# Performance work log

Hardware: AMD Instinct MI355X
Metric: run time of the kernel (lower is better)

## Reference

```python
import jax, jax.numpy as jnp
import numpy as np
import math

S, B, D = 2048, 8, 256
HEADS = 8
DPROJ = 128
DFF = 1024
DH = DPROJ // HEADS  # 16


def _layernorm(x, g, b, eps=1e-5):
    mu = jnp.mean(x, axis=-1, keepdims=True)
    var = jnp.mean((x - mu) ** 2, axis=-1, keepdims=True)
    return (x - mu) * jax.lax.rsqrt(var + eps) * g + b


def setup_inputs() -> dict:
    key = jax.random.key(0)
    ks = jax.random.split(key, 16)
    s = 0.02
    return {
        "src": jax.random.normal(ks[0], (S, B, D), dtype=jnp.float32),
        "Wq": jax.random.normal(ks[1], (D, DPROJ), dtype=jnp.float32) * s,
        "bq": jnp.zeros((DPROJ,), dtype=jnp.float32),
        "Wk": jax.random.normal(ks[2], (D, DPROJ), dtype=jnp.float32) * s,
        "bk": jnp.zeros((DPROJ,), dtype=jnp.float32),
        "Wv": jax.random.normal(ks[3], (D, DPROJ), dtype=jnp.float32) * s,
        "bv": jnp.zeros((DPROJ,), dtype=jnp.float32),
        "Wo": jax.random.normal(ks[4], (DPROJ, D), dtype=jnp.float32) * s,
        "ln1_g": jnp.ones((D,), dtype=jnp.float32),
        "ln1_b": jnp.zeros((D,), dtype=jnp.float32),
        "W1": jax.random.normal(ks[5], (D, DFF), dtype=jnp.float32) * s,
        "b1": jnp.zeros((DFF,), dtype=jnp.float32),
        "W2": jax.random.normal(ks[6], (DFF, D), dtype=jnp.float32) * s,
        "b2": jnp.zeros((D,), dtype=jnp.float32),
        "ln2_g": jnp.ones((D,), dtype=jnp.float32),
        "ln2_b": jnp.zeros((D,), dtype=jnp.float32),
    }


def reference(src, Wq, bq, Wk, bk, Wv, bv, Wo, ln1_g, ln1_b, W1, b1, W2, b2, ln2_g, ln2_b):
    # src: (S, B, D)
    q = src @ Wq + bq  # (S, B, DPROJ)
    k = src @ Wk + bk
    v = src @ Wv + bv

    # _reshape_to_batches: (S, B, h*dh) -> (S, B*h, dh), then sdpa moves batch first
    def split_heads(x):
        return jnp.transpose(x.reshape(S, B * HEADS, DH), (1, 0, 2))  # (B*h, S, dh)

    qh, kh, vh = split_heads(q), split_heads(k), split_heads(v)
    scores = jnp.einsum('bid,bjd->bij', qh, kh) / math.sqrt(DH)  # (B*h, S, S)
    attn = jax.nn.softmax(scores, axis=-1)
    ctx = jnp.einsum('bij,bjd->bid', attn, vh)  # (B*h, S, dh)

    # _reshape_from_batches: (B*h, S, dh) -> (S, B, DPROJ)
    ctx = jnp.transpose(ctx, (1, 0, 2)).reshape(S, B, DPROJ)
    y = ctx @ Wo  # (S, B, D), no bias

    x = _layernorm(src + y, ln1_g, ln1_b)
    ffn = jax.nn.relu(x @ W1 + b1) @ W2 + b2
    return _layernorm(x + ffn, ln2_g, ln2_b)
```

## Files before the change

kernel.cpp:

```cpp
#include <hip/hip_runtime.h>
#include <math.h>

#define SLEN 2048
#define BATCH 8
#define DMODEL 256
#define HEADS 8
#define DPROJ 128
#define DFF 1024
#define DH 16
#define MROWS (SLEN*BATCH)

typedef unsigned short u16;
typedef unsigned int u32;
typedef __attribute__((ext_vector_type(8))) short short8;
typedef __attribute__((ext_vector_type(4))) float f32x4;
typedef __attribute__((ext_vector_type(4))) unsigned short u16x4;

__device__ __forceinline__ u16 f2bf(float x) {
    union { float f; u32 u; } v; v.f = x;
    u32 r = v.u + 0x7FFFu + ((v.u >> 16) & 1u);
    return (u16)(r >> 16);
}
__device__ __forceinline__ float bf2f(u16 h) {
    union { u32 u; float f; } v; v.u = ((u32)h) << 16;
    return v.f;
}
__device__ __forceinline__ float fexp2(float x) { return __builtin_amdgcn_exp2f(x); }
__device__ __forceinline__ u32 pack_bf(float lo, float hi) {
    union { float f; u32 u; } a, b; a.f = lo; b.f = hi;
    return __builtin_amdgcn_perm(b.u, a.u, 0x07060302u);
}
__device__ __forceinline__ void gld16(const u16* g, u16* l) {
    __builtin_amdgcn_global_load_lds(
        (const __attribute__((address_space(1))) void*)g,
        (__attribute__((address_space(3))) void*)l, 16, 0, 0);
}

__global__ void prep_kernel(const float* __restrict__ src, u16* __restrict__ srcb,
                            const float* __restrict__ Wq, const float* __restrict__ Wk,
                            const float* __restrict__ Wv, const float* __restrict__ Wo,
                            const float* __restrict__ W1, const float* __restrict__ W2,
                            u16* __restrict__ WqT, u16* __restrict__ WkT,
                            u16* __restrict__ WvT, u16* __restrict__ WoT,
                            u16* __restrict__ W1T, u16* __restrict__ W2T) {
    if (blockIdx.x < 4096) {
        int idx = (blockIdx.x * 256 + threadIdx.x) * 4;
        float4 v = *(const float4*)(src + idx);
        u16x4 o;
        o.x = f2bf(v.x); o.y = f2bf(v.y); o.z = f2bf(v.z); o.w = f2bf(v.w);
        *(u16x4*)(srcb + idx) = o;
        return;
    }
    int i = (blockIdx.x - 4096) * 256 + threadIdx.x;
    if (i < 32768) {
        int n = i >> 8, k = i & 255;
        WqT[i] = f2bf(Wq[k * 128 + n]);
    } else if (i < 65536) {
        int j = i - 32768; int n = j >> 8, k = j & 255;
        WkT[j] = f2bf(Wk[k * 128 + n]);
    } else if (i < 98304) {
        int j = i - 65536; int n = j >> 8, k = j & 255;
        WvT[j] = f2bf(Wv[k * 128 + n]);
    } else if (i < 131072) {
        int j = i - 98304; int n = j >> 7, k = j & 127;
        WoT[j] = f2bf(Wo[k * 256 + n]);
    } else if (i < 393216) {
        int j = i - 131072; int n = j >> 8, k = j & 255;
        W1T[j] = f2bf(W1[k * 1024 + n]);
    } else if (i < 655360) {
        int j = i - 393216; int n = j >> 10, k = j & 1023;
        W2T[j] = f2bf(W2[k * 256 + n]);
    }
}

template<int BN, bool RELU, bool HAS_BIAS, bool OUT_BF16>
__global__ void mfma_gemm(const u16* __restrict__ A, const u16* __restrict__ BT,
                          const float* __restrict__ bias, void* __restrict__ Cout,
                          int M, int N, int K) {
    constexpr int NJ = BN / 32;
    __shared__ __align__(16) u16 As[128 * 32];
    __shared__ __align__(16) u16 Bs[BN * 32];
    const int tid = threadIdx.x;
    const int row0 = blockIdx.x * 128;
    const int col0 = blockIdx.y * BN;
    const int w = tid >> 6, l = tid & 63;
    const int wr = (w & 1) * 64, wc = (w >> 1) * (BN / 2);
    const int lcol = l & 15, lrow = (l >> 4) * 4, g = l >> 4;
    const int sl = l >> 2;
    const int swc = ((l & 3) ^ (sl & 3)) * 8;
    const int fsw = (g ^ (lcol & 3)) * 8;

    const u16* Ag0 = A + (size_t)(row0 + 16 * w + sl) * K + swc;
    const u16* Ag1 = Ag0 + (size_t)64 * K;
    const u16* Bg0 = BT + (size_t)(col0 + 16 * w + sl) * K + swc;
    const u16* Bg1 = Bg0 + (size_t)64 * K;
    u16* lA0 = As + (16 * w) * 32;
    u16* lA1 = As + (16 * w + 64) * 32;
    u16* lB0 = Bs + (16 * w) * 32;
    u16* lB1 = Bs + (16 * w + 64) * 32;

    f32x4 acc[4][NJ] = {};
    for (int k0 = 0; k0 < K; k0 += 32) {
        gld16(Ag0 + k0, lA0);
        gld16(Ag1 + k0, lA1);
        gld16(Bg0 + k0, lB0);
        if (BN == 128) gld16(Bg1 + k0, lB1);
        __syncthreads();
        short8 af[4], bf[NJ];
        #pragma unroll
        for (int i = 0; i < 4; ++i)
            af[i] = *(const short8*)(As + (wr + i * 16 + lcol) * 32 + fsw);
        #pragma unroll
        for (int j = 0; j < NJ; ++j)
            bf[j] = *(const short8*)(Bs + (wc + j * 16 + lcol) * 32 + fsw);
        #pragma unroll
        for (int i = 0; i < 4; ++i)
            #pragma unroll
            for (int j = 0; j < NJ; ++j)
                acc[i][j] = __builtin_amdgcn_mfma_f32_16x16x32_bf16(
                    af[i], bf[j], acc[i][j], 0, 0, 0);
        __syncthreads();
    }
    float bv[NJ];
    #pragma unroll
    for (int j = 0; j < NJ; ++j)
        bv[j] = HAS_BIAS ? bias[col0 + wc + j * 16 + lcol] : 0.f;
    #pragma unroll
    for (int i = 0; i < 4; ++i) {
        #pragma unroll
        for (int r = 0; r < 4; ++r) {
            size_t grow = row0 + wr + i * 16 + lrow + r;
            #pragma unroll
            for (int j = 0; j < NJ; ++j) {
                int gcol = col0 + wc + j * 16 + lcol;
                float c = acc[i][j][r] + bv[j];
                if (RELU) c = fmaxf(c, 0.f);
                if (OUT_BF16) ((u16*)Cout)[grow * N + gcol] = f2bf(c);
                else          ((float*)Cout)[grow * N + gcol] = c;
            }
        }
    }
}

__global__ void qkv_mfma(const u16* __restrict__ A,
                         const u16* __restrict__ WqT, const u16* __restrict__ WkT,
                         const u16* __restrict__ WvT,
                         const float* __restrict__ bq, const float* __restrict__ bk,
                         const float* __restrict__ bv,
                         u16* __restrict__ qhp, u16* __restrict__ khp,
                         u16* __restrict__ vhb) {
    const int which = blockIdx.z;
    const u16* BT   = which == 0 ? WqT : (which == 1 ? WkT : WvT);
    const float* bs = which == 0 ? bq : (which == 1 ? bk : bv);
    const float scale = which == 0 ? 0.25f * 1.44269504f : 1.0f;
    __shared__ __align__(16) u16 As[128 * 32];
    __shared__ __align__(16) u16 Bs[128 * 32];
    const int tid = threadIdx.x;
    const int row0 = blockIdx.x * 128;
    const int w = tid >> 6, l = tid & 63;
    const int wr = (w & 1) * 64, wc = (w >> 1) * 64;
    const int lcol = l & 15, lrow = (l >> 4) * 4, g = l >> 4;
    const int sl = l >> 2;
    const int swc = ((l & 3) ^ (sl & 3)) * 8;
    const int fsw = (g ^ (lcol & 3)) * 8;

    const u16* Ag0 = A + (size_t)(row0 + 16 * w + sl) * DMODEL + swc;
    const u16* Ag1 = Ag0 + (size_t)64 * DMODEL;
    const u16* Bg0 = BT + (size_t)(16 * w + sl) * DMODEL + swc;
    const u16* Bg1 = Bg0 + (size_t)64 * DMODEL;
    u16* lA0 = As + (16 * w) * 32;
    u16* lA1 = As + (16 * w + 64) * 32;
    u16* lB0 = Bs + (16 * w) * 32;
    u16* lB1 = Bs + (16 * w + 64) * 32;

    f32x4 acc[4][4] = {};
    for (int k0 = 0; k0 < DMODEL; k0 += 32) {
        gld16(Ag0 + k0, lA0);
        gld16(Ag1 + k0, lA1);
        gld16(Bg0 + k0, lB0);
        gld16(Bg1 + k0, lB1);
        __syncthreads();
        short8 af[4], bf[4];
        #pragma unroll
        for (int i = 0; i < 4; ++i)
            af[i] = *(const short8*)(As + (wr + i * 16 + lcol) * 32 + fsw);
        #pragma unroll
        for (int j = 0; j < 4; ++j)
            bf[j] = *(const short8*)(Bs + (wc + j * 16 + lcol) * 32 + fsw);
        #pragma unroll
        for (int i = 0; i < 4; ++i)
            #pragma unroll
            for (int j = 0; j < 4; ++j)
                acc[i][j] = __builtin_amdgcn_mfma_f32_16x16x32_bf16(
                    af[i], bf[j], acc[i][j], 0, 0, 0);
        __syncthreads();
    }
    #pragma unroll
    for (int i = 0; i < 4; ++i) {
        #pragma unroll
        for (int r = 0; r < 4; ++r) {
            int grow = row0 + wr + i * 16 + lrow + r;
            int b = grow & 7, s = grow >> 3;
            #pragma unroll
            for (int j = 0; j < 4; ++j) {
                int gcol = wc + j * 16 + lcol;
                int h = gcol >> 4, d = gcol & 15;
                float c = acc[i][j][r] + bs[gcol];
                if (which == 2) {
                    vhb[((size_t)(b * 8 + h) * SLEN + s) * 16 + d] = f2bf(c);
                } else {
                    u16* base = (which == 0 ? qhp : khp)
                              + ((size_t)(b * 8 + h) * SLEN + s) * 32;
                    base[d] = f2bf(c * scale);
                    base[d + 16] = 0;
                }
            }
        }
    }
}

__global__ void transpose_v(const u16* __restrict__ vhb, u16* __restrict__ vT) {
    __shared__ u16 T[128 * 24];
    const int bh = blockIdx.y;
    const int c0 = blockIdx.x * 128;
    const int t = threadIdx.x;
    {
        int key = t >> 1, half = t & 1;
        *(uint4*)(T + key * 24 + half * 8) =
            *(const uint4*)(vhb + ((size_t)bh * SLEN + c0 + key) * 16 + half * 8);
    }
    __syncthreads();
    int d = t >> 4, k8 = (t & 15) * 8;
    u16x4 o0, o1;
    o0.x = T[(k8 + 0) * 24 + d]; o0.y = T[(k8 + 1) * 24 + d];
    o0.z = T[(k8 + 2) * 24 + d]; o0.w = T[(k8 + 3) * 24 + d];
    o1.x = T[(k8 + 4) * 24 + d]; o1.y = T[(k8 + 5) * 24 + d];
    o1.z = T[(k8 + 6) * 24 + d]; o1.w = T[(k8 + 7) * 24 + d];
    u16* dst = vT + ((size_t)bh * 16 + d) * SLEN + c0 + k8;
    *(u16x4*)dst = o0;
    *(u16x4*)(dst + 4) = o1;
}

__global__ __launch_bounds__(256, 4)
void attn_mfma(const u16* __restrict__ qg, const u16* __restrict__ kg,
               const u16* __restrict__ vT, u16* __restrict__ ctx) {
    __shared__ __align__(16) u16 Ps[2 * 4 * 32 * 76];
    const int bh = blockIdx.y;
    const int q0 = blockIdx.x * 128;
    const int tid = threadIdx.x;
    const int w = tid >> 6, l = tid & 63;
    const int qc = l & 15, g = l >> 4;
    u16* Pw0 = Ps + w * 2432;
    u16* Pw1 = Ps + 9728 + w * 2432;

    short8 qf[2];
    {
        const u16* qbase = qg + ((size_t)bh * SLEN + q0 + w * 32) * 32;
        qf[0] = *(const short8*)(qbase + qc * 32 + 8 * g);
        qf[1] = *(const short8*)(qbase + (16 + qc) * 32 + 8 * g);
    }
    const u16* kbase = kg + (size_t)bh * SLEN * 32;
    const u16* vbase = vT + ((size_t)bh * 16 + qc) * SLEN;

    f32x4 o_[2] = {};
    f32x4 ls[2] = {};
    const short one_bf = (short)0x3F80;
    short8 onesB = {one_bf, one_bf, one_bf, one_bf, one_bf, one_bf, one_bf, one_bf};

    #pragma unroll 2
    for (int kt = 0; kt < 32; ++kt) {
        const int k0 = kt * 64;
        u16* Pw = (kt & 1) ? Pw1 : Pw0;
        short8 kf[4], vf[2];
        #pragma unroll
        for (int kj = 0; kj < 4; ++kj)
            kf[kj] = *(const short8*)(kbase + (size_t)(k0 + kj * 16 + qc) * 32 + 8 * g);
        #pragma unroll
        for (int ks = 0; ks < 2; ++ks)
            vf[ks] = *(const short8*)(vbase + k0 + ks * 32 + 8 * g);

        f32x4 s_[4][2];
        #pragma unroll
        for (int kj = 0; kj < 4; ++kj)
            #pragma unroll
            for (int mi = 0; mi < 2; ++mi) {
                f32x4 z = {0.f, 0.f, 0.f, 0.f};
                s_[kj][mi] = __builtin_amdgcn_mfma_f32_16x16x32_bf16(
                    kf[kj], qf[mi], z, 0, 0, 0);
            }
        #pragma unroll
        for (int mi = 0; mi < 2; ++mi)
            #pragma unroll
            for (int kj = 0; kj < 4; ++kj) {
                f32x4 sv = s_[kj][mi];
                uint2 dd;
                dd.x = pack_bf(fexp2(sv[0]), fexp2(sv[1]));
                dd.y = pack_bf(fexp2(sv[2]), fexp2(sv[3]));
                *(uint2*)(Pw + (mi * 16 + qc) * 76 + kj * 16 + 4 * g) = dd;
            }
        #pragma unroll
        for (int ks = 0; ks < 2; ++ks) {
            #pragma unroll
            for (int mi = 0; mi < 2; ++mi) {
                const u16* rp = Pw + (mi * 16 + qc) * 76 + ks * 32 + 8 * g;
                union { uint2 q[2]; short8 v; } ap;
                ap.q[0] = *(const uint2*)rp;
                ap.q[1] = *(const uint2*)(rp + 4);
                o_[mi] = __builtin_amdgcn_mfma_f32_16x16x32_bf16(ap.v, vf[ks], o_[mi], 0, 0, 0);
                ls[mi] = __builtin_amdgcn_mfma_f32_16x16x32_bf16(ap.v, onesB, ls[mi], 0, 0, 0);
            }
        }
    }
    const int b = bh >> 3, h = bh & 7;
    #pragma unroll
    for (int mi = 0; mi < 2; ++mi)
        #pragma unroll
        for (int r = 0; r < 4; ++r) {
            int qrow = q0 + w * 32 + mi * 16 + 4 * g + r;
            ctx[((size_t)qrow * BATCH + b) * DPROJ + h * DH + qc] =
                f2bf(o_[mi][r] / ls[mi][r]);
        }
}

__global__ void ln1_kernel(const float* __restrict__ src, const u16* __restrict__ y,
                           const float* __restrict__ g, const float* __restrict__ bb,
                           u16* __restrict__ xb) {
    const int w = threadIdx.x >> 6, l = threadIdx.x & 63;
    const int row = blockIdx.x * 4 + w;
    const int c = l * 4;
    size_t base = (size_t)row * DMODEL;
    float4 s4 = *(const float4*)(src + base + c);
    u16x4 y4 = *(const u16x4*)(y + base + c);
    float v[4] = { s4.x + bf2f(y4.x), s4.y + bf2f(y4.y),
                   s4.z + bf2f(y4.z), s4.w + bf2f(y4.w) };
    float sum = v[0] + v[1] + v[2] + v[3];
    float ss  = v[0]*v[0] + v[1]*v[1] + v[2]*v[2] + v[3]*v[3];
    #pragma unroll
    for (int off = 1; off < 64; off <<= 1) {
        sum += __shfl_xor(sum, off);
        ss  += __shfl_xor(ss, off);
    }
    float mu = sum * (1.0f / 256.0f);
    float var = ss * (1.0f / 256.0f) - mu * mu;
    float rs = rsqrtf(var + 1e-5f);
    float4 g4 = *(const float4*)(g + c);
    float4 b4 = *(const float4*)(bb + c);
    u16x4 o;
    o.x = f2bf((v[0] - mu) * rs * g4.x + b4.x);
    o.y = f2bf((v[1] - mu) * rs * g4.y + b4.y);
    o.z = f2bf((v[2] - mu) * rs * g4.z + b4.z);
    o.w = f2bf((v[3] - mu) * rs * g4.w + b4.w);
    *(u16x4*)(xb + base + c) = o;
}

__global__ void ln2_kernel(const u16* __restrict__ x, const u16* __restrict__ f,
                           const float* __restrict__ g, const float* __restrict__ bb,
                           float* __restrict__ out) {
    const int w = threadIdx.x >> 6, l = threadIdx.x & 63;
    const int row = blockIdx.x * 4 + w;
    const int c = l * 4;
    size_t base = (size_t)row * DMODEL;
    u16x4 x4 = *(const u16x4*)(x + base + c);
    u16x4 f4 = *(const u16x4*)(f + base + c);
    float v[4] = { bf2f(x4.x) + bf2f(f4.x), bf2f(x4.y) + bf2f(f4.y),
                   bf2f(x4.z) + bf2f(f4.z), bf2f(x4.w) + bf2f(f4.w) };
    float sum = v[0] + v[1] + v[2] + v[3];
    float ss  = v[0]*v[0] + v[1]*v[1] + v[2]*v[2] + v[3]*v[3];
    #pragma unroll
    for (int off = 1; off < 64; off <<= 1) {
        sum += __shfl_xor(sum, off);
        ss  += __shfl_xor(ss, off);
    }
    float mu = sum * (1.0f / 256.0f);
    float var = ss * (1.0f / 256.0f) - mu * mu;
    float rs = rsqrtf(var + 1e-5f);
    float4 g4 = *(const float4*)(g + c);
    float4 b4 = *(const float4*)(bb + c);
    float4 o;
    o.x = (v[0] - mu) * rs * g4.x + b4.x;
    o.y = (v[1] - mu) * rs * g4.y + b4.y;
    o.z = (v[2] - mu) * rs * g4.z + b4.z;
    o.w = (v[3] - mu) * rs * g4.w + b4.w;
    *(float4*)(out + base + c) = o;
}

extern "C" void kernel_launch(void* const* d_in, const int* in_sizes, int n_in,
                              void* d_out, int out_size, void* d_ws, size_t ws_size,
                              hipStream_t stream) {
    const float* src = (const float*)d_in[0];
    const float* Wq  = (const float*)d_in[1];
    const float* bq  = (const float*)d_in[2];
    const float* Wk  = (const float*)d_in[3];
    const float* bk  = (const float*)d_in[4];
    const float* Wv  = (const float*)d_in[5];
    const float* bv  = (const float*)d_in[6];
    const float* Wo  = (const float*)d_in[7];
    const float* g1  = (const float*)d_in[8];
    const float* be1 = (const float*)d_in[9];
    const float* W1  = (const float*)d_in[10];
    const float* b1  = (const float*)d_in[11];
    const float* W2  = (const float*)d_in[12];
    const float* b2  = (const float*)d_in[13];
    const float* g2  = (const float*)d_in[14];
    const float* be2 = (const float*)d_in[15];
    char* ws = (char*)d_ws;
    float* out = (float*)d_out;

    u16* qhp  = (u16*)(ws + 0);
    u16* khp  = (u16*)(ws + 8388608);
    u16* vhb  = (u16*)(ws + 16777216);
    u16* vT   = (u16*)(ws + 20971520);
    u16* ctxb = (u16*)(ws + 25165824);
    u16* yb   = (u16*)(ws + 29360128);
    u16* hb   = (u16*)(ws + 0);
    u16* xb   = (u16*)(ws + 37748736);
    u16* fb   = (u16*)(ws + 46137344);
    u16* srcb = (u16*)(ws + 54525952);
    u16* WqT  = (u16*)(ws + 62914560);
    u16* WkT  = (u16*)(ws + 62980096);
    u16* WvT  = (u16*)(ws + 63045632);
    u16* WoT  = (u16*)(ws + 63111168);
    u16* W1T  = (u16*)(ws + 63176704);
    u16* W2T  = (u16*)(ws + 63700992);

    prep_kernel<<<6656, 256, 0, stream>>>(src, srcb, Wq, Wk, Wv, Wo, W1, W2,
                                          WqT, WkT, WvT, WoT, W1T, W2T);
    qkv_mfma<<<dim3(128, 1, 3), 256, 0, stream>>>(srcb, WqT, WkT, WvT,
                                                  bq, bk, bv, qhp, khp, vhb);
    transpose_v<<<dim3(16, 64), 256, 0, stream>>>(vhb, vT);
    attn_mfma<<<dim3(16, 64), 256, 0, stream>>>(qhp, khp, vT, ctxb);
    mfma_gemm<64, false, false, true><<<dim3(128, 4), 256, 0, stream>>>(
        ctxb, WoT, nullptr, yb, MROWS, DMODEL, DPROJ);
    ln1_kernel<<<MROWS / 4, 256, 0, stream>>>(src, yb, g1, be1, xb);
    mfma_gemm<128, true, true, true><<<dim3(128, 8), 256, 0, stream>>>(
        xb, W1T, b1, hb, MROWS, DFF, DMODEL);
    mfma_gemm<64, false, true, true><<<dim3(128, 4), 256, 0, stream>>>(
        hb, W2T, b2, fb, MROWS, DMODEL, DFF);
    ln2_kernel<<<MROWS / 4, 256, 0, stream>>>(xb, fb, g2, be2, out);
}
```

Measured before the change: 233.4 us.

## Stage K/V tiles through double-buffered swizzled LDS with async global loads

The attention kernel now loads each 64-key K tile and the matching V^T tile into shared memory through gld16 (presumably direct global-to-LDS loads), double-buffered so the next tile's load overlaps compute on the current one. Fragments are read back from LDS with XOR swizzles to avoid bank conflicts. Previously each wave read K and V fragments straight from global memory, so the four waves fetched the same data redundantly. The P scratch buffer drops from double to single buffering, and a block-wide barrier is added every iteration, which adds sync cost and serialises the P write/read reuse.

```diff
diff --git a/kernel.cpp b/kernel.cpp
--- a/kernel.cpp
+++ b/kernel.cpp
@@ -244,14 +244,15 @@
 __global__ __launch_bounds__(256, 4)
 void attn_mfma(const u16* __restrict__ qg, const u16* __restrict__ kg,
                const u16* __restrict__ vT, u16* __restrict__ ctx) {
-    __shared__ __align__(16) u16 Ps[2 * 4 * 32 * 76];
+    __shared__ __align__(16) u16 Ks[2][64 * 32];
+    __shared__ __align__(16) u16 Vs[2][16 * 64];
+    __shared__ __align__(16) u16 Ps[4 * 32 * 76];
     const int bh = blockIdx.y;
     const int q0 = blockIdx.x * 128;
     const int tid = threadIdx.x;
     const int w = tid >> 6, l = tid & 63;
     const int qc = l & 15, g = l >> 4;
-    u16* Pw0 = Ps + w * 2432;
-    u16* Pw1 = Ps + 9728 + w * 2432;
+    u16* Pw = Ps + w * 2432;
 
     short8 qf[2];
     {
@@ -259,34 +260,54 @@
         qf[0] = *(const short8*)(qbase + qc * 32 + 8 * g);
         qf[1] = *(const short8*)(qbase + (16 + qc) * 32 + 8 * g);
     }
-    const u16* kbase = kg + (size_t)bh * SLEN * 32;
-    const u16* vbase = vT + ((size_t)bh * 16 + qc) * SLEN;
+
+    const int sl = l >> 2;
+    const int swc = ((l & 3) ^ (sl & 3)) * 8;
+    const u16* Kg = kg + (size_t)bh * SLEN * 32 + (size_t)(16 * w + sl) * 32 + swc;
+    u16* lK = (u16*)Ks + (16 * w) * 32;
+    const int vr = l >> 3, vc = l & 7;
+    const int vsw = (vc ^ (vr & 7)) * 8;
+    const u16* Vg0 = vT + ((size_t)bh * 16 + vr) * SLEN + vsw;
+    const u16* Vg1 = vT + ((size_t)bh * 16 + 8 + vr) * SLEN + vsw;
+    const int fsw = (g ^ (qc & 3)) * 8;
+    const int vf0 = ((0 * 4 + g) ^ (qc & 7)) * 8;
+    const int vf1 = ((1 * 4 + g) ^ (qc & 7)) * 8;
 
     f32x4 o_[2] = {};
     f32x4 ls[2] = {};
     const short one_bf = (short)0x3F80;
     short8 onesB = {one_bf, one_bf, one_bf, one_bf, one_bf, one_bf, one_bf, one_bf};
 
-    #pragma unroll 2
-    for (int kt = 0; kt < 32; ++kt) {
-        const int k0 = kt * 64;
-        u16* Pw = (kt & 1) ? Pw1 : Pw0;
+    gld16(Kg, lK);
+    if (w == 0) gld16(Vg0, (u16*)Vs);
+    if (w == 1) gld16(Vg1, (u16*)Vs + 8 * 64);
+    __syncthreads();
+
+    int cur = 0;
+    for (int t = 0; t < 32; ++t) {
+        if (t + 1 < 32) {
+            const int kn = (t + 1) * 64;
+            gld16(Kg + (size_t)kn * 32, lK + (cur ^ 1) * (64 * 32));
+            if (w == 0) gld16(Vg0 + kn, (u16*)Vs + (cur ^ 1) * (16 * 64));
+            if (w == 1) gld16(Vg1 + kn, (u16*)Vs + (cur ^ 1) * (16 * 64) + 8 * 64);
+        }
+        const u16* Kc = Ks[cur];
+        const u16* Vc = Vs[cur];
         short8 kf[4], vf[2];
         #pragma unroll
         for (int kj = 0; kj < 4; ++kj)
-            kf[kj] = *(const short8*)(kbase + (size_t)(k0 + kj * 16 + qc) * 32 + 8 * g);
-        #pragma unroll
-        for (int ks = 0; ks < 2; ++ks)
-            vf[ks] = *(const short8*)(vbase + k0 + ks * 32 + 8 * g);
+            kf[kj] = *(const short8*)(Kc + (kj * 16 + qc) * 32 + fsw);
+        vf[0] = *(const short8*)(Vc + qc * 64 + vf0);
+        vf[1] = *(const short8*)(Vc + qc * 64 + vf1);
 
         f32x4 s_[4][2];
         #pragma unroll
         for (int kj = 0; kj < 4; ++kj)
             #pragma unroll
             for (int mi = 0; mi < 2; ++mi) {
-                f32x4 z = {0.f, 0.f, 0.f, 0.f};
+                f32x4 zz = {0.f, 0.f, 0.f, 0.f};
                 s_[kj][mi] = __builtin_amdgcn_mfma_f32_16x16x32_bf16(
-                    kf[kj], qf[mi], z, 0, 0, 0);
+                    kf[kj], qf[mi], zz, 0, 0, 0);
             }
         #pragma unroll
         for (int mi = 0; mi < 2; ++mi)
@@ -310,7 +331,10 @@
                 ls[mi] = __builtin_amdgcn_mfma_f32_16x16x32_bf16(ap.v, onesB, ls[mi], 0, 0, 0);
             }
         }
-    }
+        __syncthreads();
+        cur ^= 1;
+    }
+
     const int b = bh >> 3, h = bh & 7;
     #pragma unroll
     for (int mi = 0; mi < 2; ++mi)
```

Measured after the change: 216.4 us. -7.3%, faster.
